# Optimization experiments

Measured on AMD Instinct MI355X. Metric: run time of the kernel, lower is better.

## Reference

```python
import jax, jax.numpy as jnp
import numpy as np

EPSILON = 0.001
PROXIMITY_THRESHOLD = 0.15


def setup_inputs() -> dict:
    key = jax.random.key(0)
    k1, k2, k3 = jax.random.split(key, 3)
    B, N, E = 8, 512, 4096
    node_positions = jax.random.uniform(k1, (B, N, 2), dtype=jnp.float32)
    adjacency = jax.random.normal(k2, (B, N, N), dtype=jnp.float32)
    edge_index = jax.random.randint(k3, (2, E), 0, B * N, dtype=jnp.int64)
    return {"node_positions": node_positions, "adjacency": adjacency, "edge_index": edge_index}


def _candidate_mask(pos, src, dst, batch, prox):
    # pos: (BN,2); src/dst/batch: (E,)
    p_src = pos[src]
    p_dst = pos[dst]
    mid = (p_src + p_dst) * 0.5                      # (E,2)
    half = jnp.linalg.norm(p_dst - p_src, axis=-1) * 0.5  # (E,)
    dist = jnp.linalg.norm(mid[:, None] - mid[None, :], axis=-1)  # (E,E)
    reach = half[:, None] + half[None, :] + prox
    E = src.shape[0]
    idx = jnp.arange(E)
    upper = idx[None, :] > idx[:, None]              # ei < ej
    same_batch = batch[:, None] == batch[None, :]
    shares = ((src[:, None] == src[None, :]) | (src[:, None] == dst[None, :])
              | (dst[:, None] == src[None, :]) | (dst[:, None] == dst[None, :]))
    return (dist < reach) & upper & same_batch & ~shares


def _segment_distance_dense(p_src, p_dst):
    # All-pairs closest-approach distance between segments i and j.
    d1 = p_dst - p_src                               # (E,2)
    sq = jnp.maximum((d1 * d1).sum(-1), 1e-12)       # (E,)
    a = sq[:, None]                                  # a_i
    e = sq[None, :]                                  # e_j
    b = d1 @ d1.T                                    # (E,E) d1_i . d1_j
    d1_dot_a1 = (d1 * p_src).sum(-1)                 # (E,) d1_k . a1_k
    c = d1_dot_a1[:, None] - d1 @ p_src.T            # d1_i . (a1_i - b1_j)
    f = p_src @ d1.T - d1_dot_a1[None, :]            # d1_j . (a1_i - b1_j)
    denom = jnp.maximum(a * e - b * b, 1e-12)
    s = (b * f - c * e) / denom
    t = (a * f - b * c) / denom
    s = jnp.clip(s, 0.0, 1.0)
    t = jnp.clip(t, 0.0, 1.0)
    t = jnp.clip((b * s + f) / e, 0.0, 1.0)
    s = jnp.clip((b * t - c) / a, 0.0, 1.0)
    closest_a = p_src[:, None, :] + s[..., None] * d1[:, None, :]   # (E,E,2)
    closest_b = p_src[None, :, :] + t[..., None] * d1[None, :, :]   # (E,E,2)
    return jnp.linalg.norm(closest_a - closest_b, axis=-1)          # (E,E)


def reference(node_positions, adjacency, edge_index):
    # adjacency is accepted (per the torch forward signature) but unused by this axiom.
    B, N, _ = node_positions.shape
    pos = node_positions.reshape(-1, 2)              # (B*N, 2)
    src = edge_index[0]
    dst = edge_index[1]
    batch = src // N                                 # (E,) batch membership per edge
    mask = jax.lax.stop_gradient(
        _candidate_mask(jax.lax.stop_gradient(pos), src, dst, batch, PROXIMITY_THRESHOLD))
    dmin = _segment_distance_dense(pos[src], pos[dst])  # (E,E)
    pair_loss = jax.nn.relu(EPSILON - dmin) * mask.astype(dmin.dtype)
    n_pairs = mask.sum()
    loss = pair_loss.sum() / jnp.maximum(n_pairs, 1).astype(dmin.dtype)
    violation_mask = mask & (pair_loss > 0)
    violation_scores = jax.lax.stop_gradient(pair_loss)
    return loss, violation_mask, violation_scores
```

## Files before the change

kernel.cpp:

```cpp
#include <hip/hip_runtime.h>


#define EDGES   4096
#define LOGE    12
#define EPS     0.001f
#define PROX    0.15f
#define NBUCKET 2048
#define ITILE   8
#define JBLK    512

__global__ __launch_bounds__(256) void edge_pre(
    const float2* __restrict__ pos,
    const int*    __restrict__ esrc,
    const int*    __restrict__ edst,
    float4* __restrict__ rec1, float4* __restrict__ rec2, float4* __restrict__ rec3)
{
#pragma clang fp contract(off)
    const int e = blockIdx.x * 256 + threadIdx.x;
    const int s = esrc[e], d = edst[e];
    const float2 a1 = pos[s], a2 = pos[d];
    const float d1x = a2.x - a1.x, d1y = a2.y - a1.y;
    const float midx = (a1.x + a2.x) * 0.5f, midy = (a1.y + a2.y) * 0.5f;
    const float half = sqrtf(d1x * d1x + d1y * d1y) * 0.5f;
    const float sq   = fmaxf(d1x * d1x + d1y * d1y, 1e-12f);
    const float dda  = d1x * a1.x + d1y * a1.y;
    rec1[e] = make_float4(a1.x, a1.y, d1x, d1y);
    rec2[e] = make_float4(midx, midy, half, dda);
    rec3[e] = make_float4(sq, __int_as_float(s), __int_as_float(d), 0.0f);
}

__device__ __forceinline__ void pair_math(
    const float4 r1i, const float4 r2i, const float4 r3i,
    const float4 r1j, const float4 r2j, const float4 r3j,
    const bool upper, float& pl, bool& mask)
{
#pragma clang fp contract(off)
    const float dmx  = r2i.x - r2j.x, dmy = r2i.y - r2j.y;
    const float dist = sqrtf(dmx * dmx + dmy * dmy);
    const float reach = r2i.z + r2j.z + PROX;

    const int si = __float_as_int(r3i.y), di_ = __float_as_int(r3i.z);
    const int sj = __float_as_int(r3j.y), dj  = __float_as_int(r3j.z);
    const bool sameb  = (si >> 9) == (sj >> 9);
    const bool shares = (si == sj) | (si == dj) | (di_ == sj) | (di_ == dj);
    mask = (dist < reach) & upper & sameb & (!shares);

    const float sqi = r3i.x, sqj = r3j.x;
    const float b = r1i.z * r1j.z + r1i.w * r1j.w;
    const float c = r2i.w - (r1i.z * r1j.x + r1i.w * r1j.y);
    const float f = (r1i.x * r1j.z + r1i.y * r1j.w) - r2j.w;
    const float denom = fmaxf(sqi * sqj - b * b, 1e-12f);

    float s = (b * f - c * sqj) / denom;
    s = fminf(fmaxf(s, 0.0f), 1.0f);
    const float t = fminf(fmaxf((b * s + f) / sqj, 0.0f), 1.0f);
    s = fminf(fmaxf((b * t - c) / sqi, 0.0f), 1.0f);

    const float cax = r1i.x + s * r1i.z, cay = r1i.y + s * r1i.w;
    const float cbx = r1j.x + t * r1j.z, cby = r1j.y + t * r1j.w;
    const float dx = cax - cbx, dy = cay - cby;
    const float dmin = sqrtf(dx * dx + dy * dy);

    pl = fmaxf(EPS - dmin, 0.0f) * (mask ? 1.0f : 0.0f);
}

__global__ __launch_bounds__(256) void pair_kernel(
    const float4* __restrict__ rec1, const float4* __restrict__ rec2,
    const float4* __restrict__ rec3,
    float*        __restrict__ out,
    float*        __restrict__ bsum,
    unsigned int* __restrict__ bcnt)
{
#pragma clang fp contract(off)
    const int ibase = blockIdx.y * ITILE;
    const int jbase = blockIdx.x * JBLK;
    const int tid   = threadIdx.x;

    float* __restrict__ o_mask  = out + 1;
    float* __restrict__ o_score = out + 1 + EDGES * EDGES;

    if (jbase + JBLK - 1 <= ibase) {
        #pragma unroll
        for (int ii = 0; ii < ITILE; ++ii) {
            const int row = (ibase + ii) << LOGE;
            o_mask [row + jbase + tid]       = 0.0f;
            o_score[row + jbase + tid]       = 0.0f;
            o_mask [row + jbase + 256 + tid] = 0.0f;
            o_score[row + jbase + 256 + tid] = 0.0f;
        }
        return;
    }

    const int j0 = jbase + tid;
    const int j1 = j0 + 256;
    const float4 r1j0 = rec1[j0], r2j0 = rec2[j0], r3j0 = rec3[j0];
    const float4 r1j1 = rec1[j1], r2j1 = rec2[j1], r3j1 = rec3[j1];

    float vsum = 0.0f;
    int   vcnt = 0;

    #pragma unroll 2
    for (int ii = 0; ii < ITILE; ++ii) {
        const int i = ibase + ii;
        const float4 r1i = rec1[i], r2i = rec2[i], r3i = rec3[i];

        float pl0, pl1; bool m0, m1;
        pair_math(r1i, r2i, r3i, r1j0, r2j0, r3j0, j0 > i, pl0, m0);
        pair_math(r1i, r2i, r3i, r1j1, r2j1, r3j1, j1 > i, pl1, m1);

        const int row = i << LOGE;
        o_mask [row + j0] = (m0 && pl0 > 0.0f) ? 1.0f : 0.0f;
        o_score[row + j0] = pl0;
        o_mask [row + j1] = (m1 && pl1 > 0.0f) ? 1.0f : 0.0f;
        o_score[row + j1] = pl1;

        vsum += pl0 + pl1;
        vcnt += (m0 ? 1 : 0) + (m1 ? 1 : 0);
    }

    #pragma unroll
    for (int off = 32; off > 0; off >>= 1) {
        vsum += __shfl_xor(vsum, off, 64);
        vcnt += __shfl_xor(vcnt, off, 64);
    }
    __shared__ float    ls[4];
    __shared__ unsigned lc[4];
    const int wid = tid >> 6, lane = tid & 63;
    if (lane == 0) { ls[wid] = vsum; lc[wid] = (unsigned)vcnt; }
    __syncthreads();
    if (tid == 0) {
        const float    s4 = ls[0] + ls[1] + ls[2] + ls[3];
        const unsigned c4 = lc[0] + lc[1] + lc[2] + lc[3];
        if (s4 != 0.0f || c4 != 0u) {
            const int bk = (blockIdx.y * 8 + blockIdx.x) & (NBUCKET - 1);
            atomicAdd(&bsum[bk], s4);
            atomicAdd(&bcnt[bk], c4);
        }
    }
}

__global__ __launch_bounds__(256) void finalize_kernel(
    const float* __restrict__ bsum, const unsigned* __restrict__ bcnt,
    float* __restrict__ out)
{
    float    s = 0.0f;
    unsigned c = 0u;
    for (int b = threadIdx.x; b < NBUCKET; b += 256) { s += bsum[b]; c += bcnt[b]; }
    #pragma unroll
    for (int off = 32; off > 0; off >>= 1) {
        s += __shfl_xor(s, off, 64);
        c += (unsigned)__shfl_xor((int)c, off, 64);
    }
    __shared__ float    ls[4];
    __shared__ unsigned lc[4];
    const int wid = threadIdx.x >> 6, lane = threadIdx.x & 63;
    if (lane == 0) { ls[wid] = s; lc[wid] = c; }
    __syncthreads();
    if (threadIdx.x == 0) {
        const float    st = ls[0] + ls[1] + ls[2] + ls[3];
        const unsigned ct = lc[0] + lc[1] + lc[2] + lc[3];
        const unsigned n  = ct > 1u ? ct : 1u;
        out[0] = st / (float)n;
    }
}

extern "C" void kernel_launch(void* const* d_in, const int* in_sizes, int n_in,
                              void* d_out, int out_size, void* d_ws, size_t ws_size,
                              hipStream_t stream) {
    const float2* pos  = (const float2*)d_in[0];
    const int*    esrc = (const int*)d_in[2];
    const int*    edst = esrc + EDGES;

    float*        out  = (float*)d_out;
    float*        bsum = (float*)d_ws;
    unsigned int* bcnt = (unsigned int*)((float*)d_ws + NBUCKET);
    float4*       rec1 = (float4*)((char*)d_ws + NBUCKET * 8);
    float4*       rec2 = rec1 + EDGES;
    float4*       rec3 = rec2 + EDGES;

    hipMemsetAsync(d_ws, 0, NBUCKET * 2 * sizeof(float), stream);

    edge_pre<<<EDGES / 256, 256, 0, stream>>>(pos, esrc, edst, rec1, rec2, rec3);
    dim3 grid(EDGES / JBLK, EDGES / ITILE);
    pair_kernel<<<grid, 256, 0, stream>>>(rec1, rec2, rec3, out, bsum, bcnt);
    finalize_kernel<<<1, 256, 0, stream>>>(bsum, bcnt, out);
}
```

Baseline: 181.8 us.

## Compact candidate pairs into a worklist before segment-distance math

Splits the pair kernel into a mask pass that zero-fills both outputs and compacts candidate (i,j) pairs into a global worklist via ballot/LDS and an atomic offset, and a second kernel that computes closest-approach distance only for listed pairs. The goal is to avoid the divisions and square roots for the large majority of pairs that fail the batch or proximity test. The pair count is taken from the worklist counter. It adds an extra kernel, a worklist buffer, and gathered loads in the second pass.

```diff
diff --git a/kernel.cpp b/kernel.cpp
--- a/kernel.cpp
+++ b/kernel.cpp
@@ -29,47 +29,11 @@
     rec3[e] = make_float4(sq, __int_as_float(s), __int_as_float(d), 0.0f);
 }
 
-__device__ __forceinline__ void pair_math(
-    const float4 r1i, const float4 r2i, const float4 r3i,
-    const float4 r1j, const float4 r2j, const float4 r3j,
-    const bool upper, float& pl, bool& mask)
-{
-#pragma clang fp contract(off)
-    const float dmx  = r2i.x - r2j.x, dmy = r2i.y - r2j.y;
-    const float dist = sqrtf(dmx * dmx + dmy * dmy);
-    const float reach = r2i.z + r2j.z + PROX;
-
-    const int si = __float_as_int(r3i.y), di_ = __float_as_int(r3i.z);
-    const int sj = __float_as_int(r3j.y), dj  = __float_as_int(r3j.z);
-    const bool sameb  = (si >> 9) == (sj >> 9);
-    const bool shares = (si == sj) | (si == dj) | (di_ == sj) | (di_ == dj);
-    mask = (dist < reach) & upper & sameb & (!shares);
-
-    const float sqi = r3i.x, sqj = r3j.x;
-    const float b = r1i.z * r1j.z + r1i.w * r1j.w;
-    const float c = r2i.w - (r1i.z * r1j.x + r1i.w * r1j.y);
-    const float f = (r1i.x * r1j.z + r1i.y * r1j.w) - r2j.w;
-    const float denom = fmaxf(sqi * sqj - b * b, 1e-12f);
-
-    float s = (b * f - c * sqj) / denom;
-    s = fminf(fmaxf(s, 0.0f), 1.0f);
-    const float t = fminf(fmaxf((b * s + f) / sqj, 0.0f), 1.0f);
-    s = fminf(fmaxf((b * t - c) / sqi, 0.0f), 1.0f);
-
-    const float cax = r1i.x + s * r1i.z, cay = r1i.y + s * r1i.w;
-    const float cbx = r1j.x + t * r1j.z, cby = r1j.y + t * r1j.w;
-    const float dx = cax - cbx, dy = cay - cby;
-    const float dmin = sqrtf(dx * dx + dy * dy);
-
-    pl = fmaxf(EPS - dmin, 0.0f) * (mask ? 1.0f : 0.0f);
-}
-
-__global__ __launch_bounds__(256) void pair_kernel(
-    const float4* __restrict__ rec1, const float4* __restrict__ rec2,
-    const float4* __restrict__ rec3,
+__global__ __launch_bounds__(256) void mask_zero_compact(
+    const float4* __restrict__ rec2, const float4* __restrict__ rec3,
     float*        __restrict__ out,
-    float*        __restrict__ bsum,
-    unsigned int* __restrict__ bcnt)
+    unsigned*     __restrict__ gcount,
+    unsigned*     __restrict__ wl)
 {
 #pragma clang fp contract(off)
     const int ibase = blockIdx.y * ITILE;
@@ -79,87 +43,127 @@
     float* __restrict__ o_mask  = out + 1;
     float* __restrict__ o_score = out + 1 + EDGES * EDGES;
 
-    if (jbase + JBLK - 1 <= ibase) {
-        #pragma unroll
-        for (int ii = 0; ii < ITILE; ++ii) {
-            const int row = (ibase + ii) << LOGE;
-            o_mask [row + jbase + tid]       = 0.0f;
-            o_score[row + jbase + tid]       = 0.0f;
-            o_mask [row + jbase + 256 + tid] = 0.0f;
-            o_score[row + jbase + 256 + tid] = 0.0f;
+    const int j0 = jbase + tid;
+    const int j1 = j0 + 256;
+
+    #pragma unroll
+    for (int ii = 0; ii < ITILE; ++ii) {
+        const int row = (ibase + ii) << LOGE;
+        o_mask [row + j0] = 0.0f;  o_mask [row + j1] = 0.0f;
+        o_score[row + j0] = 0.0f;  o_score[row + j1] = 0.0f;
+    }
+    if (jbase + JBLK - 1 <= ibase) return;
+
+    __shared__ unsigned lds_list[4][1024];
+    const int wid  = tid >> 6, lane = tid & 63;
+    const unsigned long long ltmask = (1ull << lane) - 1ull;
+
+    const float4 r2j0 = rec2[j0], r3j0 = rec3[j0];
+    const float4 r2j1 = rec2[j1], r3j1 = rec3[j1];
+    const int sj0 = __float_as_int(r3j0.y), dj0 = __float_as_int(r3j0.z);
+    const int sj1 = __float_as_int(r3j1.y), dj1 = __float_as_int(r3j1.z);
+
+    unsigned wcount = 0;
+
+    #pragma unroll
+    for (int ii = 0; ii < ITILE; ++ii) {
+        const int i = ibase + ii;
+        const float4 r2i = rec2[i], r3i = rec3[i];
+        const int si = __float_as_int(r3i.y), di = __float_as_int(r3i.z);
+
+        {
+            const float dmx = r2i.x - r2j0.x, dmy = r2i.y - r2j0.y;
+            const float dist  = sqrtf(dmx * dmx + dmy * dmy);
+            const float reach = r2i.z + r2j0.z + PROX;
+            const bool shares = (si == sj0) | (si == dj0) | (di == sj0) | (di == dj0);
+            const bool m = (dist < reach) & (j0 > i) & ((si >> 9) == (sj0 >> 9)) & (!shares);
+            const unsigned long long b = __ballot(m);
+            if (m) lds_list[wid][wcount + __popcll(b & ltmask)] = (unsigned)((i << LOGE) | j0);
+            wcount += (unsigned)__popcll(b);
         }
-        return;
+        {
+            const float dmx = r2i.x - r2j1.x, dmy = r2i.y - r2j1.y;
+            const float dist  = sqrtf(dmx * dmx + dmy * dmy);
+            const float reach = r2i.z + r2j1.z + PROX;
+            const bool shares = (si == sj1) | (si == dj1) | (di == sj1) | (di == dj1);
+            const bool m = (dist < reach) & (j1 > i) & ((si >> 9) == (sj1 >> 9)) & (!shares);
+            const unsigned long long b = __ballot(m);
+            if (m) lds_list[wid][wcount + __popcll(b & ltmask)] = (unsigned)((i << LOGE) | j1);
+            wcount += (unsigned)__popcll(b);
+        }
     }
 
-    const int j0 = jbase + tid;
-    const int j1 = j0 + 256;
-    const float4 r1j0 = rec1[j0], r2j0 = rec2[j0], r3j0 = rec3[j0];
-    const float4 r1j1 = rec1[j1], r2j1 = rec2[j1], r3j1 = rec3[j1];
+    unsigned base0 = 0;
+    if (lane == 0 && wcount) base0 = atomicAdd(gcount, wcount);
+    base0 = (unsigned)__shfl((int)base0, 0, 64);
+    for (unsigned u = lane; u < wcount; u += 64) wl[base0 + u] = lds_list[wid][u];
+}
+
+__global__ __launch_bounds__(256) void seg_kernel(
+    const float4* __restrict__ rec1, const float4* __restrict__ rec2,
+    const float4* __restrict__ rec3,
+    const unsigned* __restrict__ gcount, const unsigned* __restrict__ wl,
+    float* __restrict__ out, float* __restrict__ bsum)
+{
+#pragma clang fp contract(off)
+    const unsigned n = *gcount;
+    float* __restrict__ o_mask  = out + 1;
+    float* __restrict__ o_score = out + 1 + EDGES * EDGES;
 
     float vsum = 0.0f;
-    int   vcnt = 0;
+    for (unsigned idx = blockIdx.x * 256 + threadIdx.x; idx < n; idx += gridDim.x * 256) {
+        const unsigned k = wl[idx];
+        const int i = (int)(k >> LOGE), j = (int)(k & (EDGES - 1));
+        const float4 r1i = rec1[i], r2i = rec2[i], r3i = rec3[i];
+        const float4 r1j = rec1[j], r2j = rec2[j], r3j = rec3[j];
 
-    #pragma unroll 2
-    for (int ii = 0; ii < ITILE; ++ii) {
-        const int i = ibase + ii;
-        const float4 r1i = rec1[i], r2i = rec2[i], r3i = rec3[i];
+        const float sqi = r3i.x, sqj = r3j.x;
+        const float b = r1i.z * r1j.z + r1i.w * r1j.w;
+        const float c = r2i.w - (r1i.z * r1j.x + r1i.w * r1j.y);
+        const float f = (r1i.x * r1j.z + r1i.y * r1j.w) - r2j.w;
+        const float denom = fmaxf(sqi * sqj - b * b, 1e-12f);
 
-        float pl0, pl1; bool m0, m1;
-        pair_math(r1i, r2i, r3i, r1j0, r2j0, r3j0, j0 > i, pl0, m0);
-        pair_math(r1i, r2i, r3i, r1j1, r2j1, r3j1, j1 > i, pl1, m1);
+        float s = (b * f - c * sqj) / denom;
+        s = fminf(fmaxf(s, 0.0f), 1.0f);
+        const float t = fminf(fmaxf((b * s + f) / sqj, 0.0f), 1.0f);
+        s = fminf(fmaxf((b * t - c) / sqi, 0.0f), 1.0f);
 
-        const int row = i << LOGE;
-        o_mask [row + j0] = (m0 && pl0 > 0.0f) ? 1.0f : 0.0f;
-        o_score[row + j0] = pl0;
-        o_mask [row + j1] = (m1 && pl1 > 0.0f) ? 1.0f : 0.0f;
-        o_score[row + j1] = pl1;
+        const float cax = r1i.x + s * r1i.z, cay = r1i.y + s * r1i.w;
+        const float cbx = r1j.x + t * r1j.z, cby = r1j.y + t * r1j.w;
+        const float dx = cax - cbx, dy = cay - cby;
+        const float dmin = sqrtf(dx * dx + dy * dy);
 
-        vsum += pl0 + pl1;
-        vcnt += (m0 ? 1 : 0) + (m1 ? 1 : 0);
+        const float pl = fmaxf(EPS - dmin, 0.0f);
+        if (pl > 0.0f) {
+            o_mask[k]  = 1.0f;
+            o_score[k] = pl;
+            vsum += pl;
+        }
     }
 
     #pragma unroll
-    for (int off = 32; off > 0; off >>= 1) {
-        vsum += __shfl_xor(vsum, off, 64);
-        vcnt += __shfl_xor(vcnt, off, 64);
-    }
-    __shared__ float    ls[4];
-    __shared__ unsigned lc[4];
-    const int wid = tid >> 6, lane = tid & 63;
-    if (lane == 0) { ls[wid] = vsum; lc[wid] = (unsigned)vcnt; }
-    __syncthreads();
-    if (tid == 0) {
-        const float    s4 = ls[0] + ls[1] + ls[2] + ls[3];
-        const unsigned c4 = lc[0] + lc[1] + lc[2] + lc[3];
-        if (s4 != 0.0f || c4 != 0u) {
-            const int bk = (blockIdx.y * 8 + blockIdx.x) & (NBUCKET - 1);
-            atomicAdd(&bsum[bk], s4);
-            atomicAdd(&bcnt[bk], c4);
-        }
-    }
+    for (int off = 32; off > 0; off >>= 1) vsum += __shfl_xor(vsum, off, 64);
+    const int wid = threadIdx.x >> 6, lane = threadIdx.x & 63;
+    if (lane == 0 && vsum != 0.0f)
+        atomicAdd(&bsum[(blockIdx.x * 4 + wid) & (NBUCKET - 1)], vsum);
 }
 
 __global__ __launch_bounds__(256) void finalize_kernel(
-    const float* __restrict__ bsum, const unsigned* __restrict__ bcnt,
+    const float* __restrict__ bsum, const unsigned* __restrict__ gcount,
     float* __restrict__ out)
 {
-    float    s = 0.0f;
-    unsigned c = 0u;
-    for (int b = threadIdx.x; b < NBUCKET; b += 256) { s += bsum[b]; c += bcnt[b]; }
+    float s = 0.0f;
+    for (int b = threadIdx.x; b < NBUCKET; b += 256) s += bsum[b];
     #pragma unroll
-    for (int off = 32; off > 0; off >>= 1) {
-        s += __shfl_xor(s, off, 64);
-        c += (unsigned)__shfl_xor((int)c, off, 64);
-    }
-    __shared__ float    ls[4];
-    __shared__ unsigned lc[4];
+    for (int off = 32; off > 0; off >>= 1) s += __shfl_xor(s, off, 64);
+    __shared__ float ls[4];
     const int wid = threadIdx.x >> 6, lane = threadIdx.x & 63;
-    if (lane == 0) { ls[wid] = s; lc[wid] = c; }
+    if (lane == 0) ls[wid] = s;
     __syncthreads();
     if (threadIdx.x == 0) {
-        const float    st = ls[0] + ls[1] + ls[2] + ls[3];
-        const unsigned ct = lc[0] + lc[1] + lc[2] + lc[3];
-        const unsigned n  = ct > 1u ? ct : 1u;
+        const float st = ls[0] + ls[1] + ls[2] + ls[3];
+        const unsigned ct = *gcount;
+        const unsigned n = ct > 1u ? ct : 1u;
         out[0] = st / (float)n;
     }
 }
@@ -171,17 +175,20 @@
     const int*    esrc = (const int*)d_in[2];
     const int*    edst = esrc + EDGES;
 
-    float*        out  = (float*)d_out;
-    float*        bsum = (float*)d_ws;
-    unsigned int* bcnt = (unsigned int*)((float*)d_ws + NBUCKET);
-    float4*       rec1 = (float4*)((char*)d_ws + NBUCKET * 8);
-    float4*       rec2 = rec1 + EDGES;
-    float4*       rec3 = rec2 + EDGES;
+    float*    out    = (float*)d_out;
+    char*     ws     = (char*)d_ws;
+    unsigned* gcount = (unsigned*)ws;
+    float*    bsum   = (float*)(ws + 1024);
+    unsigned* wl     = (unsigned*)(ws + (1u << 20));
+    float4*   rec1   = (float4*)(ws + (256u << 20));
+    float4*   rec2   = rec1 + EDGES;
+    float4*   rec3   = rec2 + EDGES;
 
-    hipMemsetAsync(d_ws, 0, NBUCKET * 2 * sizeof(float), stream);
+    hipMemsetAsync(d_ws, 0, 16384, stream);
 
     edge_pre<<<EDGES / 256, 256, 0, stream>>>(pos, esrc, edst, rec1, rec2, rec3);
     dim3 grid(EDGES / JBLK, EDGES / ITILE);
-    pair_kernel<<<grid, 256, 0, stream>>>(rec1, rec2, rec3, out, bsum, bcnt);
-    finalize_kernel<<<1, 256, 0, stream>>>(bsum, bcnt, out);
+    mask_zero_compact<<<grid, 256, 0, stream>>>(rec2, rec3, out, gcount, wl);
+    seg_kernel<<<512, 256, 0, stream>>>(rec1, rec2, rec3, gcount, wl, out, bsum);
+    finalize_kernel<<<1, 256, 0, stream>>>(bsum, gcount, out);
 }
```

New measurement: 248.2 us. 36.6% more time.
